# Performance work log

Measured on AMD Instinct MI355X. Metric: run time of the kernel, lower is better.

The kernel has to match this reference:

```python
import jax, jax.numpy as jnp
import numpy as np

ROPE_BASE = 10000
B, L, D, NH = 2, 2048, 1024, 16
HD = D // NH


def apply_rope(inputs, positions, base_frequency):
    # inputs: [B, L, N, H], positions: [L]
    head_dim = inputs.shape[-1]
    fraction = 2 * jnp.arange(0, head_dim // 2) / head_dim
    timescale = base_frequency ** fraction  # [H/2]
    sinusoid = positions[..., None] / timescale[None, None, :]  # [1, L, H/2]
    sinusoid = sinusoid[..., None, :]  # [1, L, 1, H/2]
    sin, cos = jnp.sin(sinusoid), jnp.cos(sinusoid)
    first, second = jnp.split(inputs, 2, axis=-1)
    out = jnp.concatenate([first * cos - second * sin,
                           second * cos + first * sin], axis=-1)
    return out.astype(inputs.dtype)


def setup_inputs() -> dict:
    key = jax.random.key(0)
    ks = jax.random.split(key, 5)
    s = 0.02
    return {
        "x": jax.random.normal(ks[0], (B, L, D), jnp.float32),
        "wq_w": jax.random.normal(ks[1], (D, D), jnp.float32) * s,
        "wq_b": jnp.zeros((D,), jnp.float32),
        "wk_w": jax.random.normal(ks[2], (D, D), jnp.float32) * s,
        "wk_b": jnp.zeros((D,), jnp.float32),
        "wv_w": jax.random.normal(ks[3], (D, D), jnp.float32) * s,
        "wv_b": jnp.zeros((D,), jnp.float32),
        "wo_w": jax.random.normal(ks[4], (D, D), jnp.float32) * s,
        "wo_b": jnp.zeros((D,), jnp.float32),
    }


def reference(x, wq_w, wq_b, wk_w, wk_b, wv_w, wv_b, wo_w, wo_b):
    b, l, _ = x.shape
    q = (x @ wq_w + wq_b).reshape(b, l, NH, HD)
    k = (x @ wk_w + wk_b).reshape(b, l, NH, HD)
    v = (x @ wv_w + wv_b).reshape(b, l, NH, HD)
    pos = jnp.arange(l)
    q = apply_rope(q, pos, ROPE_BASE)
    k = apply_rope(k, pos, ROPE_BASE)
    # [B, N, L, H]
    q = q.transpose(0, 2, 1, 3)
    k = k.transpose(0, 2, 1, 3)
    v = v.transpose(0, 2, 1, 3)
    scale = jnp.sqrt(jnp.asarray(HD, q.dtype))
    scores = jnp.einsum('bnqh,bnkh->bnqk', q, k) / scale  # [B, N, L, L]
    causal = jnp.tril(jnp.ones((l, l), bool))
    scores = jnp.where(causal, scores, jnp.finfo(scores.dtype).min)
    attn = jax.nn.softmax(scores, axis=-1)
    ctx = jnp.einsum('bnqk,bnkh->bnqh', attn, v)
    ctx = ctx.transpose(0, 2, 1, 3).reshape(b, l, D)
    return ctx @ wo_w + wo_b
```

## Files before the change

### kernel.cpp

```cpp
#include <hip/hip_runtime.h>
#include <hip/hip_bf16.h>
#include <float.h>
#include <math.h>

#define BB  2
#define LLEN 2048
#define DD  1024
#define NHH 16
#define HDD 64
#define MROWS (BB * LLEN)

typedef __bf16 bf16x8  __attribute__((ext_vector_type(8)));
typedef float  f32x4   __attribute__((ext_vector_type(4)));
typedef float  f32x16  __attribute__((ext_vector_type(16)));
typedef ushort us8     __attribute__((ext_vector_type(8)));

#define EXP2F(x) __builtin_amdgcn_exp2f(x)

static __device__ __forceinline__ ushort f2bf(float f) {
    __hip_bfloat16 h = __float2bfloat16(f);
    return *reinterpret_cast<ushort*>(&h);
}
static __device__ __forceinline__ float bfu(ushort u) {
    unsigned x = (unsigned)u << 16;
    return __uint_as_float(x);
}
static __device__ __forceinline__ unsigned pack2(float a, float b) {
    return (unsigned)f2bf(a) | ((unsigned)f2bf(b) << 16);
}

__device__ __forceinline__ void gload16(const void* g, void* l) {
    __builtin_amdgcn_global_load_lds(
        (const __attribute__((address_space(1))) void*)g,
        (__attribute__((address_space(3))) void*)l, 16, 0, 0);
}

__global__ __launch_bounds__(256) void cvt_x_k(const float* __restrict__ in,
                                               ushort* __restrict__ out) {
    int idx = blockIdx.x * 256 + threadIdx.x;
    float4 v = reinterpret_cast<const float4*>(in)[idx];
    ushort4 o;
    o.x = f2bf(v.x); o.y = f2bf(v.y); o.z = f2bf(v.z); o.w = f2bf(v.w);
    reinterpret_cast<ushort4*>(out)[idx] = o;
}

__global__ __launch_bounds__(256) void wt_cvt_all_k(const float* __restrict__ w0,
                                                    const float* __restrict__ w1,
                                                    const float* __restrict__ w2,
                                                    const float* __restrict__ w3,
                                                    ushort* __restrict__ qkv,
                                                    ushort* __restrict__ wo) {
    __shared__ float T[64][65];
    const int z = blockIdx.z;
    const float* in = (z == 0) ? w0 : (z == 1) ? w1 : (z == 2) ? w2 : w3;
    ushort* out = (z < 3) ? (qkv + (size_t)z * 1024 * DD) : wo;

    const int r0 = blockIdx.y * 64, c0 = blockIdx.x * 64;
    const int tid = threadIdx.x;
    for (int i = tid; i < 64 * 16; i += 256) {
        int r = i >> 4, c4 = (i & 15) * 4;
        float4 v = *reinterpret_cast<const float4*>(&in[(size_t)(r0 + r) * DD + c0 + c4]);
        T[r][c4 + 0] = v.x; T[r][c4 + 1] = v.y; T[r][c4 + 2] = v.z; T[r][c4 + 3] = v.w;
    }
    __syncthreads();
    for (int i = tid; i < 64 * 16; i += 256) {
        int rr = i >> 4, cc4 = (i & 15) * 4;
        ushort4 o;
        o.x = f2bf(T[cc4 + 0][rr]);
        o.y = f2bf(T[cc4 + 1][rr]);
        o.z = f2bf(T[cc4 + 2][rr]);
        o.w = f2bf(T[cc4 + 3][rr]);
        *reinterpret_cast<ushort4*>(&out[(size_t)(c0 + rr) * DD + r0 + cc4]) = o;
    }
}

template <int MODE>
__global__ __launch_bounds__(256) void gemm_mfma_k(
    const __bf16* __restrict__ A, const __bf16* __restrict__ Bt,
    const float* __restrict__ bias0, const float* __restrict__ bias1,
    const float* __restrict__ bias2,
    float* __restrict__ out_f32,
    __hip_bfloat16* __restrict__ oq, __hip_bfloat16* __restrict__ ok,
    __hip_bfloat16* __restrict__ ov) {
    constexpr int K = DD;
    __shared__ char smem[32768];
    __bf16* As = (__bf16*)smem;
    __bf16* Bs = As + 128 * 64;

    const int tid  = threadIdx.x;
    const int w    = tid >> 6;
    const int lane = tid & 63;
    const int lr   = lane & 15;
    const int lg   = lane >> 4;
    const int wr   = w >> 1, wc = w & 1;
    const int bm = blockIdx.y * 128, bn = blockIdx.x * 128;

    const int srow = lane >> 3;
    const int scol = ((lane & 7) ^ srow) * 8;
    const __bf16* gA = A  + (size_t)(bm + w * 32 + srow) * K + scol;
    const __bf16* gB = Bt + (size_t)(bn + w * 32 + srow) * K + scol;
    char* ldsA = (char*)As + w * 32 * 128;
    char* ldsB = (char*)Bs + w * 32 * 128;

    f32x4 acc[4][4] = {};

    const int l7 = lr & 7;
    for (int k0 = 0; k0 < K; k0 += 64) {
#pragma unroll
        for (int c = 0; c < 4; ++c) {
            gload16(gA + (size_t)(c * 8) * K + k0, ldsA + c * 1024);
            gload16(gB + (size_t)(c * 8) * K + k0, ldsB + c * 1024);
        }
        __syncthreads();
#pragma unroll
        for (int kk = 0; kk < 2; ++kk) {
            bf16x8 a[4], b[4];
#pragma unroll
            for (int m = 0; m < 4; ++m)
                a[m] = *reinterpret_cast<const bf16x8*>(
                    As + (wr * 64 + m * 16 + lr) * 64 + (((kk * 4 + lg) ^ l7) << 3));
#pragma unroll
            for (int n = 0; n < 4; ++n)
                b[n] = *reinterpret_cast<const bf16x8*>(
                    Bs + (wc * 64 + n * 16 + lr) * 64 + (((kk * 4 + lg) ^ l7) << 3));
#pragma unroll
            for (int m = 0; m < 4; ++m)
#pragma unroll
                for (int n = 0; n < 4; ++n)
                    acc[m][n] = __builtin_amdgcn_mfma_f32_16x16x32_bf16(a[m], b[n], acc[m][n], 0, 0, 0);
        }
        __syncthreads();
    }

    if (MODE == 1) {
        const int seg = bn >> 10;
        const int colbase = (bn & 1023) + wc * 64;
        const int h = colbase >> 6;
        if (seg == 2) {
#pragma unroll
            for (int n = 0; n < 4; ++n) {
                const int hd = n * 16 + lr;
                const float bv = bias2[colbase + hd];
#pragma unroll
                for (int m = 0; m < 4; ++m) {
                    const int rowb = bm + wr * 64 + m * 16 + lg * 4;
                    const int b = rowb >> 11, l0 = rowb & (LLEN - 1);
                    ushort4 st;
                    st.x = f2bf(acc[m][n][0] + bv);
                    st.y = f2bf(acc[m][n][1] + bv);
                    st.z = f2bf(acc[m][n][2] + bv);
                    st.w = f2bf(acc[m][n][3] + bv);
                    const int bh = b * NHH + h;
                    const int t  = l0 >> 5;
                    const int j  = ((hd >> 5) << 1) | ((l0 >> 4) & 1);
                    const int ln = (hd & 31) + ((l0 >> 3) & 1) * 32;
                    const int e0 = l0 & 7;
                    size_t base = ((((size_t)bh * 64 + t) * 4 + j) * 64 + ln) * 8 + e0;
                    *reinterpret_cast<ushort4*>(&ov[base]) = st;
                }
            }
        } else {
            const float* biasp = (seg == 0) ? bias0 : bias1;
            const float osc = (seg == 0) ? 0.18033688011112042f : 1.0f;
            ushort* LP = (ushort*)smem + (size_t)w * 4096;
            __syncthreads();
#pragma unroll
            for (int n2 = 0; n2 < 2; ++n2) {
                const int d = n2 * 16 + lr;
                const float tsd = exp2f((float)d * -0.4152410118609203f);
                const float bv0 = biasp[colbase + d];
                const float bv1 = biasp[colbase + d + 32];
                const int c0  = d >> 4;
                const int hi8 = (d >> 3) & 1;
#pragma unroll
                for (int m = 0; m < 4; ++m) {
#pragma unroll
                    for (int i = 0; i < 4; ++i) {
                        const int lw = m * 16 + lg * 4 + i;
                        const int lglob = (bm & (LLEN - 1)) + wr * 64 + lw;
                        float s, c;
                        __sincosf((float)lglob * tsd, &s, &c);
                        const float x0 = acc[m][n2][i] + bv0;
                        const float x1 = acc[m][n2 + 2][i] + bv1;
                        const int tt = lw >> 5;
                        const int ln = (lw & 31) + 32 * hi8;
                        LP[(((tt << 2) + c0) * 64 + ln) * 8 + (d & 7)] =
                            f2bf((x0 * c - x1 * s) * osc);
                        LP[(((tt << 2) + c0 + 2) * 64 + ln) * 8 + (d & 7)] =
                            f2bf((x1 * c + x0 * s) * osc);
                    }
                }
            }
            __syncthreads();
            ushort* dstp = (ushort*)((seg == 0) ? oq : ok);
            const int bh0 = (bm >> 11) * NHH + h;
            const int tg0 = ((bm & (LLEN - 1)) >> 5) + wr * 2;
#pragma unroll
            for (int tt = 0; tt < 2; ++tt)
#pragma unroll
                for (int c = 0; c < 4; ++c) {
                    us8 v = *reinterpret_cast<const us8*>(
                        &LP[(((tt << 2) + c) * 64 + lane) * 8]);
                    size_t base = ((((size_t)bh0 * 64 + tg0 + tt) * 4 + c) * 64 + lane) * 8;
                    *reinterpret_cast<us8*>(&dstp[base]) = v;
                }
        }
    } else {
        float* FP = (float*)smem + (size_t)w * 2048;
#pragma unroll
        for (int ph = 0; ph < 2; ++ph) {
            __syncthreads();
#pragma unroll
            for (int m2 = 0; m2 < 2; ++m2) {
                const int m = ph * 2 + m2;
#pragma unroll
                for (int n = 0; n < 4; ++n) {
                    const int col = n * 16 + lr;
                    const float bv = bias0[bn + wc * 64 + col];
#pragma unroll
                    for (int i = 0; i < 4; ++i) {
                        const int rw = m2 * 16 + lg * 4 + i;
                        FP[rw * 64 + col] = acc[m][n][i] + bv;
                    }
                }
            }
            __syncthreads();
#pragma unroll
            for (int it = 0; it < 8; ++it) {
                const int idx = it * 64 + lane;
                const int rw = idx >> 4;
                const int cq = idx & 15;
                float4 v = *reinterpret_cast<const float4*>(&FP[rw * 64 + cq * 4]);
                const int row = bm + wr * 64 + ph * 32 + rw;
                *reinterpret_cast<float4*>(
                    &out_f32[(size_t)row * DD + bn + wc * 64 + cq * 4]) = v;
            }
        }
    }
}

#define ATTN_LOAD(KF, VF, T0)                                                   \
    do {                                                                        \
        const __bf16* kp_ = kbase + (size_t)(T0) * 2048;                        \
        KF[0] = *reinterpret_cast<const bf16x8*>(kp_);                          \
        KF[1] = *reinterpret_cast<const bf16x8*>(kp_ + 512);                    \
        KF[2] = *reinterpret_cast<const bf16x8*>(kp_ + 1024);                   \
        KF[3] = *reinterpret_cast<const bf16x8*>(kp_ + 1536);                   \
        const __bf16* vp_ = vbase + (size_t)(T0) * 2048;                        \
        VF[0] = *reinterpret_cast<const bf16x8*>(vp_);                          \
        VF[1] = *reinterpret_cast<const bf16x8*>(vp_ + 512);                    \
        VF[2] = *reinterpret_cast<const bf16x8*>(vp_ + 1024);                   \
        VF[3] = *reinterpret_cast<const bf16x8*>(vp_ + 1536);                   \
    } while (0)

#define ATTN_TILE(KF, VF, T0, MASKIT, QG)                                       \
    do {                                                                        \
        f32x16 s_ = {};                                                         \
        __builtin_amdgcn_s_setprio(1);                                          \
        s_ = __builtin_amdgcn_mfma_f32_32x32x16_bf16(KF[0], qf[0], s_, 0, 0, 0);\
        s_ = __builtin_amdgcn_mfma_f32_32x32x16_bf16(KF[1], qf[1], s_, 0, 0, 0);\
        s_ = __builtin_amdgcn_mfma_f32_32x32x16_bf16(KF[2], qf[2], s_, 0, 0, 0);\
        s_ = __builtin_amdgcn_mfma_f32_32x32x16_bf16(KF[3], qf[3], s_, 0, 0, 0);\
        __builtin_amdgcn_s_setprio(0);                                          \
        float p_[16];                                                           \
        const int k0_ = (T0) * 32;                                              \
        if (MASKIT) {                                                           \
            _Pragma("unroll")                                                   \
            for (int i = 0; i < 16; ++i) {                                      \
                int kkg_ = k0_ + (i & 3) + 8 * (i >> 2) + 4 * hi;               \
                p_[i] = (kkg_ <= (QG)) ? EXP2F(s_[i]) : 0.f;                    \
            }                                                                   \
        } else {                                                                \
            _Pragma("unroll")                                                   \
            for (int i = 0; i < 16; ++i) p_[i] = EXP2F(s_[i]);                  \
        }                                                                       \
        _Pragma("unroll")                                                       \
        for (int i = 0; i < 16; ++i) lsum += p_[i];                             \
        unsigned u_[8], x_[8];                                                  \
        _Pragma("unroll")                                                       \
        for (int j = 0; j < 8; ++j)                                             \
            u_[j] = pack2(p_[2 * j], p_[2 * j + 1]);                            \
        _Pragma("unroll")                                                       \
        for (int j = 0; j < 8; ++j)                                             \
            x_[j] = (unsigned)__shfl_xor((int)u_[j], 32);                       \
        union { unsigned d[4]; bf16x8 v; } B1_, B2_;                            \
        if (hi == 0) {                                                          \
            B1_.d[0] = u_[0]; B1_.d[1] = u_[1]; B1_.d[2] = x_[0]; B1_.d[3] = x_[1]; \
            B2_.d[0] = u_[4]; B2_.d[1] = u_[5]; B2_.d[2] = x_[4]; B2_.d[3] = x_[5]; \
        } else {                                                                \
            B1_.d[0] = x_[2]; B1_.d[1] = x_[3]; B1_.d[2] = u_[2]; B1_.d[3] = u_[3]; \
            B2_.d[0] = x_[6]; B2_.d[1] = x_[7]; B2_.d[2] = u_[6]; B2_.d[3] = u_[7]; \
        }                                                                       \
        __builtin_amdgcn_s_setprio(1);                                          \
        o0 = __builtin_amdgcn_mfma_f32_32x32x16_bf16(VF[0], B1_.v, o0, 0, 0, 0);\
        o0 = __builtin_amdgcn_mfma_f32_32x32x16_bf16(VF[1], B2_.v, o0, 0, 0, 0);\
        o1 = __builtin_amdgcn_mfma_f32_32x32x16_bf16(VF[2], B1_.v, o1, 0, 0, 0);\
        o1 = __builtin_amdgcn_mfma_f32_32x32x16_bf16(VF[3], B2_.v, o1, 0, 0, 0);\
        __builtin_amdgcn_s_setprio(0);                                          \
    } while (0)

#define ATTN_COMPUTE(QT, QG)                                                    \
    do {                                                                        \
        lsum = 0.f;                                                             \
        o0 = (f32x16){}; o1 = (f32x16){};                                       \
        const __bf16* qp_ = qbase + (size_t)(QT) * 2048;                        \
        qf[0] = *reinterpret_cast<const bf16x8*>(qp_);                          \
        qf[1] = *reinterpret_cast<const bf16x8*>(qp_ + 512);                    \
        qf[2] = *reinterpret_cast<const bf16x8*>(qp_ + 1024);                   \
        qf[3] = *reinterpret_cast<const bf16x8*>(qp_ + 1536);                   \
        bf16x8 kf[4], vf[4];                                                    \
        for (int t = w; t <= (QT); t += 4) {                                    \
            ATTN_LOAD(kf, vf, t);                                               \
            ATTN_TILE(kf, vf, t, t == (QT), QG);                                \
        }                                                                       \
    } while (0)

#define ATTN_WRITE_PARTIALS()                                                   \
    do {                                                                        \
        _Pragma("unroll")                                                       \
        for (int r = 0; r < 16; r += 2) {                                       \
            *reinterpret_cast<unsigned*>(&oLs[w][lane][r])      = pack2(o0[r], o0[r + 1]); \
            *reinterpret_cast<unsigned*>(&oLs[w][lane][16 + r]) = pack2(o1[r], o1[r + 1]); \
        }                                                                       \
        lvL[w][lane] = lsum;                                                    \
    } while (0)

#define ATTN_MERGE_WRITE(QG)                                                    \
    do {                                                                        \
        float Lt = 0.f;                                                         \
        _Pragma("unroll")                                                       \
        for (int j = 0; j < 4; ++j)                                             \
            Lt += lvL[j][q32] + lvL[j][q32 + 32];                               \
        const float inv = 1.0f / Lt;                                            \
        __hip_bfloat16* dst = ctx + ((size_t)(b * LLEN + (QG))) * DD + h * HDD; \
        const int T = w >> 1;                                                   \
        const int gb = (w & 1) * 2;                                             \
        _Pragma("unroll")                                                       \
        for (int g2 = 0; g2 < 2; ++g2) {                                        \
            const int g = gb + g2;                                              \
            const int rb = T * 16 + 4 * g;                                      \
            float acc4[4] = {0.f, 0.f, 0.f, 0.f};                               \
            _Pragma("unroll")                                                   \
            for (int j = 0; j < 4; ++j) {                                       \
                unsigned a = *reinterpret_cast<const unsigned*>(&oLs[j][lane][rb]);     \
                unsigned c = *reinterpret_cast<const unsigned*>(&oLs[j][lane][rb + 2]); \
                acc4[0] += bfu((ushort)(a & 0xffff));                           \
                acc4[1] += bfu((ushort)(a >> 16));                              \
                acc4[2] += bfu((ushort)(c & 0xffff));                           \
                acc4[3] += bfu((ushort)(c >> 16));                              \
            }                                                                   \
            ushort st4[4];                                                      \
            _Pragma("unroll")                                                   \
            for (int e = 0; e < 4; ++e) st4[e] = f2bf(acc4[e] * inv);           \
            const int d = T * 32 + 8 * g + 4 * hi;                              \
            *reinterpret_cast<ushort4*>(dst + d) =                              \
                *reinterpret_cast<ushort4*>(st4);                               \
        }                                                                       \
    } while (0)

__global__ __launch_bounds__(256) void attn_mfma16_k(const __bf16* __restrict__ Qp,
                                                     const __bf16* __restrict__ Kp,
                                                     const __bf16* __restrict__ Vp,
                                                     __hip_bfloat16* __restrict__ ctx) {
    __shared__ ushort oLs[4][64][34];
    __shared__ float lvL[4][64];

    const int tid  = threadIdx.x;
    const int w    = tid >> 6;
    const int lane = tid & 63;
    const int q32  = lane & 31;
    const int hi   = lane >> 5;

    const int bid = blockIdx.x;
    const int g_  = (bid & 7) * 128 + (bid >> 3);
    const int bh  = g_ >> 5;
    const int ap  = g_ & 31;
    const int qtA = 63 - ap;
    const int qtB = ap;
    const int qgA = qtA * 32 + q32;
    const int qgB = qtB * 32 + q32;

    const __bf16* qbase = Qp + (size_t)bh * (64 * 4 * 512) + lane * 8;
    const __bf16* kbase = Kp + (size_t)bh * (64 * 4 * 512) + lane * 8;
    const __bf16* vbase = Vp + (size_t)bh * (64 * 4 * 512) + lane * 8;

    const int b = bh >> 4, h = bh & 15;

    bf16x8 qf[4];
    f32x16 o0, o1;
    float lsum;

    ATTN_COMPUTE(qtA, qgA);
    ATTN_WRITE_PARTIALS();
    __syncthreads();
    ATTN_MERGE_WRITE(qgA);

    ATTN_COMPUTE(qtB, qgB);
    __syncthreads();
    ATTN_WRITE_PARTIALS();
    __syncthreads();
    ATTN_MERGE_WRITE(qgB);
}

extern "C" void kernel_launch(void* const* d_in, const int* in_sizes, int n_in,
                              void* d_out, int out_size, void* d_ws, size_t ws_size,
                              hipStream_t stream) {
    const float* x    = (const float*)d_in[0];
    const float* wq_w = (const float*)d_in[1];
    const float* wq_b = (const float*)d_in[2];
    const float* wk_w = (const float*)d_in[3];
    const float* wk_b = (const float*)d_in[4];
    const float* wv_w = (const float*)d_in[5];
    const float* wv_b = (const float*)d_in[6];
    const float* wo_w = (const float*)d_in[7];
    const float* wo_b = (const float*)d_in[8];
    float* out = (float*)d_out;

    const size_t MB = 1024 * 1024;
    char* p = (char*)d_ws;
    __bf16* x16   = (__bf16*)p;            p += 8 * MB;
    __bf16* wqkvt = (__bf16*)p;            p += 6 * MB;
    __bf16* wot   = (__bf16*)p;            p += 2 * MB;
    __hip_bfloat16* qp16 = (__hip_bfloat16*)p; p += 8 * MB;
    __hip_bfloat16* kp16 = (__hip_bfloat16*)p; p += 8 * MB;
    __hip_bfloat16* vp16 = (__hip_bfloat16*)p; p += 8 * MB;
    __hip_bfloat16* ctx16 = (__hip_bfloat16*)p;

    hipLaunchKernelGGL(cvt_x_k, dim3(4096), dim3(256), 0, stream, x, (ushort*)x16);
    hipLaunchKernelGGL(wt_cvt_all_k, dim3(16, 16, 4), dim3(256), 0, stream,
                       wq_w, wk_w, wv_w, wo_w, (ushort*)wqkvt, (ushort*)wot);

    hipLaunchKernelGGL((gemm_mfma_k<1>), dim3(24, 32), dim3(256), 0, stream,
                       x16, wqkvt, wq_b, wk_b, wv_b, (float*)nullptr, qp16, kp16, vp16);

    hipLaunchKernelGGL(attn_mfma16_k, dim3(1024), dim3(256), 0, stream,
                       (const __bf16*)qp16, (const __bf16*)kp16, (const __bf16*)vp16, ctx16);

    hipLaunchKernelGGL((gemm_mfma_k<0>), dim3(8, 32), dim3(256), 0, stream,
                       (const __bf16*)ctx16, wot, wo_b, (const float*)nullptr, (const float*)nullptr,
                       out, (__hip_bfloat16*)nullptr, (__hip_bfloat16*)nullptr, (__hip_bfloat16*)nullptr);
}
```

Measured before the change: 110.2 us.

## Shrink GEMM tiles to 64-row blocks for more CTAs and occupancy

Both GEMMs move from 128x128 tiles with a 2x2 warp layout to 64-row tiles. Each warp now owns 16 rows, and the tile is 128 columns wide for the QKV GEMM and 64 for the output GEMM. The launch grids grow to match and launch_bounds asks for 6 blocks per CU. The aim is to fill the many CUs with more blocks and to lower per-block register and LDS use. In exchange, data reuse per loaded tile drops (each B fragment feeds one MFMA per warp instead of four), which raises LDS read traffic and global reloads of the operands.

```diff
diff --git a/kernel.cpp b/kernel.cpp
--- a/kernel.cpp
+++ b/kernel.cpp
@@ -75,166 +75,154 @@
 }
 
 template <int MODE>
-__global__ __launch_bounds__(256) void gemm_mfma_k(
+__global__ __launch_bounds__(256, 6) void gemm_mfma_k(
     const __bf16* __restrict__ A, const __bf16* __restrict__ Bt,
     const float* __restrict__ bias0, const float* __restrict__ bias1,
     const float* __restrict__ bias2,
     float* __restrict__ out_f32,
     __hip_bfloat16* __restrict__ oq, __hip_bfloat16* __restrict__ ok,
     __hip_bfloat16* __restrict__ ov) {
-    constexpr int K = DD;
-    __shared__ char smem[32768];
+    constexpr int K  = DD;
+    constexpr int NF = (MODE == 1) ? 8 : 4;
+    constexpr int BN = NF * 16;
+    constexpr int SMEMB = (64 + BN) * 64 * 2;
+    __shared__ char smem[SMEMB];
     __bf16* As = (__bf16*)smem;
-    __bf16* Bs = As + 128 * 64;
+    __bf16* Bs = As + 64 * 64;
 
     const int tid  = threadIdx.x;
     const int w    = tid >> 6;
     const int lane = tid & 63;
     const int lr   = lane & 15;
     const int lg   = lane >> 4;
-    const int wr   = w >> 1, wc = w & 1;
-    const int bm = blockIdx.y * 128, bn = blockIdx.x * 128;
-
-    const int srow = lane >> 3;
-    const int scol = ((lane & 7) ^ srow) * 8;
-    const __bf16* gA = A  + (size_t)(bm + w * 32 + srow) * K + scol;
-    const __bf16* gB = Bt + (size_t)(bn + w * 32 + srow) * K + scol;
-    char* ldsA = (char*)As + w * 32 * 128;
-    char* ldsB = (char*)Bs + w * 32 * 128;
-
-    f32x4 acc[4][4] = {};
-
+    const int bm = blockIdx.y * 64, bn = blockIdx.x * BN;
+
+    const int srow8 = lane >> 3;
+    const int schk  = (lane & 7) ^ srow8;
+    const __bf16* gA = A  + (size_t)(bm + w * 16 + srow8) * K + schk * 8;
+    const __bf16* gB = Bt + (size_t)(bn + w * (NF * 4) + srow8) * K + schk * 8;
+    char* ldsA = (char*)As + w * 16 * 128;
+    char* ldsB = (char*)Bs + w * (NF * 4) * 128;
+
+    f32x4 acc[NF] = {};
     const int l7 = lr & 7;
+
     for (int k0 = 0; k0 < K; k0 += 64) {
 #pragma unroll
-        for (int c = 0; c < 4; ++c) {
+        for (int c = 0; c < 2; ++c)
             gload16(gA + (size_t)(c * 8) * K + k0, ldsA + c * 1024);
+#pragma unroll
+        for (int c = 0; c < NF / 2; ++c)
             gload16(gB + (size_t)(c * 8) * K + k0, ldsB + c * 1024);
-        }
         __syncthreads();
 #pragma unroll
         for (int kk = 0; kk < 2; ++kk) {
-            bf16x8 a[4], b[4];
-#pragma unroll
-            for (int m = 0; m < 4; ++m)
-                a[m] = *reinterpret_cast<const bf16x8*>(
-                    As + (wr * 64 + m * 16 + lr) * 64 + (((kk * 4 + lg) ^ l7) << 3));
-#pragma unroll
-            for (int n = 0; n < 4; ++n)
-                b[n] = *reinterpret_cast<const bf16x8*>(
-                    Bs + (wc * 64 + n * 16 + lr) * 64 + (((kk * 4 + lg) ^ l7) << 3));
-#pragma unroll
-            for (int m = 0; m < 4; ++m)
-#pragma unroll
-                for (int n = 0; n < 4; ++n)
-                    acc[m][n] = __builtin_amdgcn_mfma_f32_16x16x32_bf16(a[m], b[n], acc[m][n], 0, 0, 0);
+            const int rchk = ((kk * 4 + lg) ^ l7) << 3;
+            bf16x8 a = *reinterpret_cast<const bf16x8*>(As + (w * 16 + lr) * 64 + rchk);
+#pragma unroll
+            for (int n = 0; n < NF; ++n) {
+                bf16x8 b = *reinterpret_cast<const bf16x8*>(Bs + (n * 16 + lr) * 64 + rchk);
+                acc[n] = __builtin_amdgcn_mfma_f32_16x16x32_bf16(a, b, acc[n], 0, 0, 0);
+            }
         }
         __syncthreads();
     }
 
     if (MODE == 1) {
         const int seg = bn >> 10;
-        const int colbase = (bn & 1023) + wc * 64;
-        const int h = colbase >> 6;
+        const int colbase = bn & 1023;
+        const int h0 = colbase >> 6;
+        const int b  = bm >> 11;
+        const int bmL = bm & 2047;
         if (seg == 2) {
 #pragma unroll
-            for (int n = 0; n < 4; ++n) {
-                const int hd = n * 16 + lr;
-                const float bv = bias2[colbase + hd];
-#pragma unroll
-                for (int m = 0; m < 4; ++m) {
-                    const int rowb = bm + wr * 64 + m * 16 + lg * 4;
-                    const int b = rowb >> 11, l0 = rowb & (LLEN - 1);
-                    ushort4 st;
-                    st.x = f2bf(acc[m][n][0] + bv);
-                    st.y = f2bf(acc[m][n][1] + bv);
-                    st.z = f2bf(acc[m][n][2] + bv);
-                    st.w = f2bf(acc[m][n][3] + bv);
-                    const int bh = b * NHH + h;
-                    const int t  = l0 >> 5;
-                    const int j  = ((hd >> 5) << 1) | ((l0 >> 4) & 1);
-                    const int ln = (hd & 31) + ((l0 >> 3) & 1) * 32;
-                    const int e0 = l0 & 7;
-                    size_t base = ((((size_t)bh * 64 + t) * 4 + j) * 64 + ln) * 8 + e0;
-                    *reinterpret_cast<ushort4*>(&ov[base]) = st;
-                }
+            for (int n = 0; n < NF; ++n) {
+                const int h  = h0 + (n >> 2);
+                const int hd = (n & 3) * 16 + lr;
+                const float bv = bias2[colbase + n * 16 + lr];
+                const int rowb = bm + w * 16 + lg * 4;
+                const int l0 = rowb & 2047;
+                ushort4 st;
+                st.x = f2bf(acc[n][0] + bv);
+                st.y = f2bf(acc[n][1] + bv);
+                st.z = f2bf(acc[n][2] + bv);
+                st.w = f2bf(acc[n][3] + bv);
+                const int bh = b * NHH + h;
+                const int t  = l0 >> 5;
+                const int j  = ((hd >> 5) << 1) | ((l0 >> 4) & 1);
+                const int ln = (hd & 31) + ((l0 >> 3) & 1) * 32;
+                const int e0 = l0 & 7;
+                size_t base = ((((size_t)bh * 64 + t) * 4 + j) * 64 + ln) * 8 + e0;
+                *reinterpret_cast<ushort4*>(&ov[base]) = st;
             }
         } else {
             const float* biasp = (seg == 0) ? bias0 : bias1;
             const float osc = (seg == 0) ? 0.18033688011112042f : 1.0f;
-            ushort* LP = (ushort*)smem + (size_t)w * 4096;
-            __syncthreads();
-#pragma unroll
-            for (int n2 = 0; n2 < 2; ++n2) {
-                const int d = n2 * 16 + lr;
-                const float tsd = exp2f((float)d * -0.4152410118609203f);
-                const float bv0 = biasp[colbase + d];
-                const float bv1 = biasp[colbase + d + 32];
-                const int c0  = d >> 4;
-                const int hi8 = (d >> 3) & 1;
-#pragma unroll
-                for (int m = 0; m < 4; ++m) {
+            ushort* LP = (ushort*)smem + w * 2048;
+#pragma unroll
+            for (int hh = 0; hh < 2; ++hh) {
+#pragma unroll
+                for (int n2 = 0; n2 < 2; ++n2) {
+                    const int nA = hh * 4 + n2, nB = nA + 2;
+                    const int d  = n2 * 16 + lr;
+                    const float tsd = exp2f((float)d * -0.4152410118609203f);
+                    const float bv0 = biasp[colbase + hh * 64 + d];
+                    const float bv1 = biasp[colbase + hh * 64 + d + 32];
+                    const int c0  = d >> 4;
+                    const int hi8 = (d >> 3) & 1;
 #pragma unroll
                     for (int i = 0; i < 4; ++i) {
-                        const int lw = m * 16 + lg * 4 + i;
-                        const int lglob = (bm & (LLEN - 1)) + wr * 64 + lw;
+                        const int lw = lg * 4 + i;
+                        const int l  = bmL + w * 16 + lw;
                         float s, c;
-                        __sincosf((float)lglob * tsd, &s, &c);
-                        const float x0 = acc[m][n2][i] + bv0;
-                        const float x1 = acc[m][n2 + 2][i] + bv1;
-                        const int tt = lw >> 5;
-                        const int ln = (lw & 31) + 32 * hi8;
-                        LP[(((tt << 2) + c0) * 64 + ln) * 8 + (d & 7)] =
+                        __sincosf((float)l * tsd, &s, &c);
+                        const float x0 = acc[nA][i] + bv0;
+                        const float x1 = acc[nB][i] + bv1;
+                        const int lnL = lw + 16 * hi8;
+                        LP[hh * 1024 + (c0 * 32 + lnL) * 8 + (d & 7)] =
                             f2bf((x0 * c - x1 * s) * osc);
-                        LP[(((tt << 2) + c0 + 2) * 64 + ln) * 8 + (d & 7)] =
+                        LP[hh * 1024 + ((c0 + 2) * 32 + lnL) * 8 + (d & 7)] =
                             f2bf((x1 * c + x0 * s) * osc);
                     }
                 }
             }
             __syncthreads();
             ushort* dstp = (ushort*)((seg == 0) ? oq : ok);
-            const int bh0 = (bm >> 11) * NHH + h;
-            const int tg0 = ((bm & (LLEN - 1)) >> 5) + wr * 2;
-#pragma unroll
-            for (int tt = 0; tt < 2; ++tt)
-#pragma unroll
-                for (int c = 0; c < 4; ++c) {
-                    us8 v = *reinterpret_cast<const us8*>(
-                        &LP[(((tt << 2) + c) * 64 + lane) * 8]);
-                    size_t base = ((((size_t)bh0 * 64 + tg0 + tt) * 4 + c) * 64 + lane) * 8;
+            const int t   = (bmL >> 5) + (w >> 1);
+            const int r0w = (w & 1) * 16;
+#pragma unroll
+            for (int hh = 0; hh < 2; ++hh) {
+                const int bh = b * NHH + h0 + hh;
+#pragma unroll
+                for (int it = 0; it < 2; ++it) {
+                    const int f = it * 64 + lane;
+                    const int c = f >> 5, lnL = f & 31;
+                    const int ln = r0w + (lnL & 15) + 32 * (lnL >> 4);
+                    us8 v = *reinterpret_cast<const us8*>(&LP[hh * 1024 + f * 8]);
+                    size_t base = ((((size_t)bh * 64 + t) * 4 + c) * 64 + ln) * 8;
                     *reinterpret_cast<us8*>(&dstp[base]) = v;
                 }
+            }
         }
     } else {
-        float* FP = (float*)smem + (size_t)w * 2048;
-#pragma unroll
-        for (int ph = 0; ph < 2; ++ph) {
-            __syncthreads();
-#pragma unroll
-            for (int m2 = 0; m2 < 2; ++m2) {
-                const int m = ph * 2 + m2;
-#pragma unroll
-                for (int n = 0; n < 4; ++n) {
-                    const int col = n * 16 + lr;
-                    const float bv = bias0[bn + wc * 64 + col];
-#pragma unroll
-                    for (int i = 0; i < 4; ++i) {
-                        const int rw = m2 * 16 + lg * 4 + i;
-                        FP[rw * 64 + col] = acc[m][n][i] + bv;
-                    }
-                }
-            }
-            __syncthreads();
-#pragma unroll
-            for (int it = 0; it < 8; ++it) {
-                const int idx = it * 64 + lane;
-                const int rw = idx >> 4;
-                const int cq = idx & 15;
-                float4 v = *reinterpret_cast<const float4*>(&FP[rw * 64 + cq * 4]);
-                const int row = bm + wr * 64 + ph * 32 + rw;
-                *reinterpret_cast<float4*>(
-                    &out_f32[(size_t)row * DD + bn + wc * 64 + cq * 4]) = v;
-            }
+        float* FP = (float*)smem + w * 1024;
+        __syncthreads();
+#pragma unroll
+        for (int n = 0; n < NF; ++n) {
+            const int col = n * 16 + lr;
+            const float bv = bias0[bn + col];
+#pragma unroll
+            for (int i = 0; i < 4; ++i)
+                FP[(lg * 4 + i) * 64 + col] = acc[n][i] + bv;
+        }
+        __syncthreads();
+#pragma unroll
+        for (int it = 0; it < 4; ++it) {
+            const int f = it * 64 + lane;
+            const int row16 = f >> 4, cq = f & 15;
+            float4 v = *reinterpret_cast<const float4*>(&FP[row16 * 64 + cq * 4]);
+            const int row = bm + w * 16 + row16;
+            *reinterpret_cast<float4*>(&out_f32[(size_t)row * DD + bn + cq * 4]) = v;
         }
     }
 }
@@ -430,13 +418,13 @@
     hipLaunchKernelGGL(wt_cvt_all_k, dim3(16, 16, 4), dim3(256), 0, stream,
                        wq_w, wk_w, wv_w, wo_w, (ushort*)wqkvt, (ushort*)wot);
 
-    hipLaunchKernelGGL((gemm_mfma_k<1>), dim3(24, 32), dim3(256), 0, stream,
+    hipLaunchKernelGGL((gemm_mfma_k<1>), dim3(24, 64), dim3(256), 0, stream,
                        x16, wqkvt, wq_b, wk_b, wv_b, (float*)nullptr, qp16, kp16, vp16);
 
     hipLaunchKernelGGL(attn_mfma16_k, dim3(1024), dim3(256), 0, stream,
                        (const __bf16*)qp16, (const __bf16*)kp16, (const __bf16*)vp16, ctx16);
 
-    hipLaunchKernelGGL((gemm_mfma_k<0>), dim3(8, 32), dim3(256), 0, stream,
+    hipLaunchKernelGGL((gemm_mfma_k<0>), dim3(16, 64), dim3(256), 0, stream,
                        (const __bf16*)ctx16, wot, wo_b, (const float*)nullptr, (const float*)nullptr,
                        out, (__hip_bfloat16*)nullptr, (__hip_bfloat16*)nullptr, (__hip_bfloat16*)nullptr);
 }
```

Result: faster. 103.9 us (-5.7%).
